# Kernel tuning notes

Hardware: AMD Instinct MI355X
Metric: run time of the kernel (lower is better)

The kernel has to match this reference:

```python
import jax, jax.numpy as jnp
import numpy as np

NUM_BINS = 16
TAIL_BOUND = 3.0
MIN_BIN_WIDTH = 1e-3
MIN_BIN_HEIGHT = 1e-3
MIN_DERIVATIVE = 1e-3
DERIV_CONST = float(np.log(np.exp(1.0 - MIN_DERIVATIVE) - 1.0))  # softplus^-1(1-min_d)

FEATURES = 512
BATCH = 8192
HIDDEN = 1024


def setup_inputs() -> dict:
    key = jax.random.key(0)
    k1, k2, k3 = jax.random.split(key, 3)
    n_id = FEATURES // 2
    n_tr = FEATURES // 2
    out_dim = n_tr * (3 * NUM_BINS - 1)  # 47 params per transformed feature
    inputs = jax.random.normal(k1, (BATCH, FEATURES), jnp.float32)
    W1 = jax.random.normal(k2, (n_id, HIDDEN), jnp.float32) * (1.0 / np.sqrt(n_id))
    b1 = jnp.zeros((HIDDEN,), jnp.float32)
    W2 = jax.random.normal(k3, (HIDDEN, out_dim), jnp.float32) * (1.0 / np.sqrt(HIDDEN))
    b2 = jnp.zeros((out_dim,), jnp.float32)
    # mask = [1,0,1,0,...]: transform features at even indices, identity at odd
    transform_idx = jnp.arange(0, FEATURES, 2, dtype=jnp.int32)
    identity_idx = jnp.arange(1, FEATURES, 2, dtype=jnp.int32)
    return dict(inputs=inputs, W1=W1, b1=b1, W2=W2, b2=b2,
                identity_idx=identity_idx, transform_idx=transform_idx)


def _rq_spline_forward(x, uw, uh, ud):
    """Unconstrained (linear-tail) rational-quadratic spline, forward direction.
    x: [B, D]; uw/uh: [B, D, K]; ud: [B, D, K-1]. Returns (y, logabsdet) per-element."""
    K = NUM_BINS
    B_ = TAIL_BOUND
    inside = (x >= -B_) & (x <= B_)
    xc = jnp.clip(x, -B_, B_)  # safe values for gather/formula; masked out later

    # pad derivatives with the constant so boundary derivative == 1 (linear tails)
    pad = jnp.full(ud.shape[:-1] + (1,), DERIV_CONST, ud.dtype)
    ud = jnp.concatenate([pad, ud, pad], axis=-1)  # [B, D, K+1]

    widths = jax.nn.softmax(uw, axis=-1)
    widths = MIN_BIN_WIDTH + (1.0 - MIN_BIN_WIDTH * K) * widths
    cumw = jnp.cumsum(widths, axis=-1)
    cumw = jnp.pad(cumw, [(0, 0), (0, 0), (1, 0)])
    cumw = 2.0 * B_ * cumw - B_
    cumw = cumw.at[..., 0].set(-B_).at[..., -1].set(B_)
    widths = jnp.diff(cumw, axis=-1)

    heights = jax.nn.softmax(uh, axis=-1)
    heights = MIN_BIN_HEIGHT + (1.0 - MIN_BIN_HEIGHT * K) * heights
    cumh = jnp.cumsum(heights, axis=-1)
    cumh = jnp.pad(cumh, [(0, 0), (0, 0), (1, 0)])
    cumh = 2.0 * B_ * cumh - B_
    cumh = cumh.at[..., 0].set(-B_).at[..., -1].set(B_)
    heights = jnp.diff(cumh, axis=-1)

    derivs = MIN_DERIVATIVE + jax.nn.softplus(ud)  # [B, D, K+1]
    delta = heights / widths                        # [B, D, K]

    # data-dependent bin search (searchsorted equivalent)
    idx = jnp.clip(jnp.sum((xc[..., None] >= cumw).astype(jnp.int32), axis=-1) - 1, 0, K - 1)
    idx = idx[..., None]
    g = lambda a: jnp.take_along_axis(a, idx, axis=-1)[..., 0]

    in_cw, in_w = g(cumw), g(widths)
    in_ch, in_h = g(cumh), g(heights)
    in_delta = g(delta)
    d0 = g(derivs)
    d1 = jnp.take_along_axis(derivs, idx + 1, axis=-1)[..., 0]

    theta = (xc - in_cw) / in_w
    t1m = theta * (1.0 - theta)
    denom = in_delta + (d0 + d1 - 2.0 * in_delta) * t1m
    numer = in_h * (in_delta * theta * theta + d0 * t1m)
    y = in_ch + numer / denom
    dnum = in_delta * in_delta * (d1 * theta * theta + 2.0 * in_delta * t1m + d0 * (1.0 - theta) ** 2)
    lad = jnp.log(dnum) - 2.0 * jnp.log(denom)

    y = jnp.where(inside, y, x)          # linear tails: identity outside
    lad = jnp.where(inside, lad, 0.0)
    return y, lad


def reference(inputs, W1, b1, W2, b2, identity_idx, transform_idx):
    B = inputs.shape[0]
    n_tr = transform_idx.shape[0]
    K = NUM_BINS
    identity_split = inputs[:, identity_idx]      # [B, 256]
    transform_split = inputs[:, transform_idx]    # [B, 256]

    h = jax.nn.relu(identity_split @ W1 + b1)
    params = (h @ W2 + b2).reshape(B, n_tr, 3 * K - 1)
    uw = params[..., :K]
    uh = params[..., K:2 * K]
    ud = params[..., 2 * K:]

    y, lad = _rq_spline_forward(transform_split, uw, uh, ud)
    logabsdet = jnp.sum(lad, axis=-1)  # sum_except_batch

    outputs = jnp.zeros_like(inputs)
    outputs = outputs.at[:, identity_idx].set(identity_split)
    outputs = outputs.at[:, transform_idx].set(y)
    return outputs, logabsdet
```

## Files before the change

### kernel.cpp

```cpp
#include <hip/hip_runtime.h>

#define BATCH 8192
#define FEAT  512
#define NID   256
#define NTR   256
#define HID   1024
#define PPF   47
#define PPFP  48
#define NOUT  (NTR*PPF)
#define TBOUND 3.0f
#define MIN_W 0.001f
#define MIN_H 0.001f
#define MIN_D 0.001f

typedef __bf16 bf16x8 __attribute__((ext_vector_type(8)));
typedef float  f32x4  __attribute__((ext_vector_type(4)));

__device__ __forceinline__ unsigned short f2bf(float f) {
  unsigned u = __float_as_uint(f);
  u += 0x7FFFu + ((u >> 16) & 1u);
  return (unsigned short)(u >> 16);
}

__device__ __forceinline__ void gload16(const void* g, void* l) {
  __builtin_amdgcn_global_load_lds(
      (const __attribute__((address_space(1))) void*)g,
      (__attribute__((address_space(3))) void*)l, 16, 0, 0);
}

__global__ void k_pack_all(const float* __restrict__ in,
                           const float* __restrict__ W1,
                           const float* __restrict__ W2,
                           unsigned short* __restrict__ idbf,
                           unsigned short* __restrict__ W1T,
                           unsigned short* __restrict__ W2T,
                           float* __restrict__ outp) {
  const int bid = blockIdx.x;
  const int tid = threadIdx.x;
  if (bid < 4096) {
    int b = bid * 2 + (tid >> 7);
    int j4 = tid & 127;
    float4 v = ((const float4*)(in + (long)b * FEAT))[j4];
    ((float4*)(outp + (long)b * FEAT))[j4] = v;
    ushort2 h;
    h.x = f2bf(v.y);
    h.y = f2bf(v.w);
    ((ushort2*)(idbf + (long)b * NID))[j4] = h;
  } else if (bid < 4160) {
    __shared__ unsigned short tl[64][65];
    int i = bid - 4096;
    int n0 = (i & 15) * 64, k0 = (i >> 4) * 64;
    int c = tid & 63, r4 = tid >> 6;
    #pragma unroll
    for (int j = 0; j < 16; ++j) {
      int kk = r4 + j * 4;
      tl[kk][c] = f2bf(W1[(k0 + kk) * HID + n0 + c]);
    }
    __syncthreads();
    #pragma unroll
    for (int j = 0; j < 16; ++j) {
      int nn = r4 + j * 4;
      W1T[(n0 + nn) * NID + k0 + c] = tl[c][nn];
    }
  } else if (bid < 7168) {
    __shared__ unsigned short tl[64][65];
    int i = bid - 4160;
    int ns0 = (i % 188) * 64, k0 = (i / 188) * 64;
    int c = tid & 63, r4 = tid >> 6;
    #pragma unroll
    for (int j = 0; j < 16; ++j) {
      int kk = r4 + j * 4;
      tl[kk][c] = f2bf(W2[(k0 + kk) * (long)NOUT + ns0 + c]);
    }
    __syncthreads();
    #pragma unroll
    for (int j = 0; j < 16; ++j) {
      int nn = r4 + j * 4;
      int ns = ns0 + nn;
      int nd = (ns / PPF) * PPFP + (ns % PPF);
      W2T[(long)nd * HID + k0 + c] = tl[c][nn];
    }
  } else {
    int idx = (bid - 7168) * 256 + tid;
    int f = idx >> 10, k = idx & 1023;
    W2T[((long)(f * PPFP + PPF)) * HID + k] = 0;
  }
}

__global__ __launch_bounds__(256, 2) void k_gemm1(
    const unsigned short* __restrict__ A, const unsigned short* __restrict__ Bw,
    const float* __restrict__ b1, unsigned short* __restrict__ H) {
  __shared__ __align__(16) char sm[65536];
  const int tid = threadIdx.x;
  const int lane = tid & 63, wid = tid >> 6;
  const int c = lane & 15, g = lane >> 4;
  const int wm = wid >> 1, wn = wid & 1;
  const int m0 = blockIdx.x * 128, n0 = blockIdx.y * 128;

  f32x4 zero = {0.f, 0.f, 0.f, 0.f};
  f32x4 acc[4][4];
  #pragma unroll
  for (int a = 0; a < 4; ++a)
    #pragma unroll
    for (int b = 0; b < 4; ++b) acc[a][b] = zero;

  #define G1_STAGE(half, ks)                                                   \
    {                                                                          \
      char* bA = sm + (half) * 32768;                                          \
      char* bB = bA + 16384;                                                   \
      _Pragma("unroll")                                                        \
      for (int j = 0; j < 4; ++j) {                                            \
        int s0 = j * 256 + wid * 64;                                           \
        int s = s0 + lane;                                                     \
        int row = s >> 3, kb = (s & 7) ^ (row & 7);                            \
        gload16(A + (long)(m0 + row) * NID + (ks) * 64 + kb * 8, bA + s0 * 16);\
        gload16(Bw + (long)(n0 + row) * NID + (ks) * 64 + kb * 8, bB + s0 * 16);\
      }                                                                        \
    }

  G1_STAGE(0, 0);
  __syncthreads();
  for (int ks = 0; ks < 4; ++ks) {
    int cur = ks & 1;
    if (ks < 3) G1_STAGE(cur ^ 1, ks + 1);
    char* bA = sm + cur * 32768;
    char* bB = bA + 16384;
    #pragma unroll
    for (int kk = 0; kk < 2; ++kk) {
      bf16x8 av[4], bv[4];
      int kbl = kk * 4 + g;
      #pragma unroll
      for (int mf = 0; mf < 4; ++mf) {
        int row = wm * 64 + mf * 16 + c;
        av[mf] = *(const bf16x8*)(bA + row * 128 + ((kbl ^ (row & 7)) << 4));
      }
      #pragma unroll
      for (int nf = 0; nf < 4; ++nf) {
        int col = wn * 64 + nf * 16 + c;
        bv[nf] = *(const bf16x8*)(bB + col * 128 + ((kbl ^ (col & 7)) << 4));
      }
      #pragma unroll
      for (int mf = 0; mf < 4; ++mf)
        #pragma unroll
        for (int nf = 0; nf < 4; ++nf)
          acc[mf][nf] = __builtin_amdgcn_mfma_f32_16x16x32_bf16(
              av[mf], bv[nf], acc[mf][nf], 0, 0, 0);
    }
    __syncthreads();
  }
  #pragma unroll
  for (int nf = 0; nf < 4; ++nf) {
    float bb = b1[n0 + wn * 64 + nf * 16 + c];
    #pragma unroll
    for (int mf = 0; mf < 4; ++mf) {
      #pragma unroll
      for (int i = 0; i < 4; ++i) {
        int row = m0 + wm * 64 + mf * 16 + 4 * g + i;
        int col = n0 + wn * 64 + nf * 16 + c;
        float v = acc[mf][nf][i] + bb;
        H[(long)row * HID + col] = f2bf(fmaxf(v, 0.f));
      }
    }
  }
}

__global__ __launch_bounds__(512, 4) void k_gemm2_spline(
    const unsigned short* __restrict__ Hb, const unsigned short* __restrict__ W2T,
    const float* __restrict__ b2, const float* __restrict__ inp,
    float* __restrict__ outp, float* __restrict__ ladw) {
  __shared__ __align__(16) char sm[81920];
  const int tid = threadIdx.x;
  const int lane = tid & 63, wid = tid >> 6;
  const int c = lane & 15, g = lane >> 4;
  const int wm = wid >> 2, wn = wid & 3;
  const long m0 = (long)blockIdx.x * 128;
  const int bn = blockIdx.y;
  const int n0 = bn * 192;

  f32x4 zero = {0.f, 0.f, 0.f, 0.f};
  f32x4 acc[4][3];
  #pragma unroll
  for (int a = 0; a < 4; ++a)
    #pragma unroll
    for (int b = 0; b < 3; ++b) acc[a][b] = zero;

  const char *gA0, *gA1, *gB0, *gB1, *gB2;
  int dA0, dA1, dB0, dB1, dB2;
  {
    int s0, s, row, kb;
    s0 = wid * 64;            s = s0 + lane; row = s >> 3; kb = (s & 7) ^ (row & 7);
    gA0 = (const char*)(Hb + (m0 + row) * 1024L + kb * 8); dA0 = s0 * 16;
    s0 = 512 + wid * 64;      s = s0 + lane; row = s >> 3; kb = (s & 7) ^ (row & 7);
    gA1 = (const char*)(Hb + (m0 + row) * 1024L + kb * 8); dA1 = s0 * 16;
    s0 = wid * 64;            s = s0 + lane; row = s >> 3; kb = (s & 7) ^ (row & 7);
    gB0 = (const char*)(W2T + (long)(n0 + row) * 1024L + kb * 8); dB0 = s0 * 16 + 16384;
    s0 = 512 + wid * 64;      s = s0 + lane; row = s >> 3; kb = (s & 7) ^ (row & 7);
    gB1 = (const char*)(W2T + (long)(n0 + row) * 1024L + kb * 8); dB1 = s0 * 16 + 16384;
    s0 = 1024 + wid * 64;     s = s0 + lane; row = s >> 3; kb = (s & 7) ^ (row & 7);
    gB2 = (const char*)(W2T + (long)(n0 + row) * 1024L + kb * 8); dB2 = s0 * 16 + 16384;
  }
  int oA[2][4], oB[2][3];
  #pragma unroll
  for (int kk = 0; kk < 2; ++kk) {
    int kbl = kk * 4 + g;
    #pragma unroll
    for (int mf = 0; mf < 4; ++mf) {
      int row = wm * 64 + mf * 16 + c;
      oA[kk][mf] = row * 128 + ((kbl ^ (row & 7)) << 4);
    }
    #pragma unroll
    for (int nf = 0; nf < 3; ++nf) {
      int col = wn * 48 + nf * 16 + c;
      oB[kk][nf] = col * 128 + ((kbl ^ (col & 7)) << 4) + 16384;
    }
  }

  #define G2_STAGE(HALF, IMM)                                        \
    {                                                                \
      gload16(gA0 + (IMM), sm + (HALF) * 40960 + dA0);               \
      gload16(gA1 + (IMM), sm + (HALF) * 40960 + dA1);               \
      gload16(gB0 + (IMM), sm + (HALF) * 40960 + dB0);               \
      gload16(gB1 + (IMM), sm + (HALF) * 40960 + dB1);               \
      gload16(gB2 + (IMM), sm + (HALF) * 40960 + dB2);               \
    }

  #define G2_BUMP(N) { gA0 += (N); gA1 += (N); gB0 += (N); gB1 += (N); gB2 += (N); }

  #define G2_COMP(HALF)                                                        \
    {                                                                          \
      _Pragma("unroll")                                                        \
      for (int kk = 0; kk < 2; ++kk) {                                         \
        bf16x8 av[4], bv[3];                                                   \
        _Pragma("unroll")                                                      \
        for (int mf = 0; mf < 4; ++mf)                                         \
          av[mf] = *(const bf16x8*)(sm + (HALF) * 40960 + oA[kk][mf]);         \
        _Pragma("unroll")                                                      \
        for (int nf = 0; nf < 3; ++nf)                                         \
          bv[nf] = *(const bf16x8*)(sm + (HALF) * 40960 + oB[kk][nf]);         \
        _Pragma("unroll")                                                      \
        for (int mf = 0; mf < 4; ++mf)                                         \
          _Pragma("unroll")                                                    \
          for (int nf = 0; nf < 3; ++nf)                                       \
            acc[mf][nf] = __builtin_amdgcn_mfma_f32_16x16x32_bf16(             \
                av[mf], bv[nf], acc[mf][nf], 0, 0, 0);                         \
      }                                                                        \
    }

  G2_STAGE(0, 0);
  G2_BUMP(128);
  __syncthreads();
  for (int ks2 = 0; ks2 < 7; ++ks2) {
    G2_STAGE(1, 0);
    G2_COMP(0);
    __syncthreads();
    G2_STAGE(0, 128);
    G2_COMP(1);
    __syncthreads();
    G2_BUMP(256);
  }
  G2_STAGE(1, 0);
  G2_COMP(0);
  __syncthreads();
  G2_COMP(1);
  __syncthreads();

  float* stA = (float*)(sm + wid * 8704);
  float* stB = stA + 1088;
  const int t = bn * 4 + wn;
  const float* b2t = b2 + t * PPF;
  const float bw = b2t[c];
  const float bh = b2t[16 + c];
  const float bd = (c < 15) ? b2t[32 + c] : 0.f;
  const long r = m0 + wm * 64 + lane;
  float x = inp[r * FEAT + 2 * t];

  #pragma unroll
  for (int mf = 0; mf < 4; ++mf) {
    f32x4 vw = acc[mf][0], vh = acc[mf][1];
    #pragma unroll
    for (int i = 0; i < 4; ++i) { vw[i] += bw; vh[i] += bh; }
    *(f32x4*)(stA + c * 68 + mf * 16 + 4 * g) = vw;
    *(f32x4*)(stB + c * 68 + mf * 16 + 4 * g) = vh;
  }

  float xc = fminf(fmaxf(x, -TBOUND), TBOUND);
  int idx = 0;
  float in_cw, in_w, in_ch, in_h;
  {
    float u[16];
    #pragma unroll
    for (int k = 0; k < 16; ++k) u[k] = stA[k * 68 + lane];
    float mx = u[0];
    #pragma unroll
    for (int k = 1; k < 16; ++k) mx = fmaxf(mx, u[k]);
    float e[16], s = 0.f;
    #pragma unroll
    for (int k = 0; k < 16; ++k) { e[k] = __expf(u[k] - mx); s += e[k]; }
    float inv = (1.f - MIN_W * 16.f) / s;
    float wk = fmaf(e[0], inv, MIN_W);
    float wsel = wk, cum = 0.f;
    in_cw = -TBOUND;
    #pragma unroll
    for (int k = 0; k < 15; ++k) {
      cum += wk;
      float knot = fmaf(2.f * TBOUND, cum, -TBOUND);
      float wk1 = fmaf(e[k + 1], inv, MIN_W);
      bool le = (knot <= xc);
      idx = le ? k + 1 : idx;
      in_cw = le ? knot : in_cw;
      wsel = le ? wk1 : wsel;
      wk = wk1;
    }
    in_w = 2.f * TBOUND * wsel;
  }
  #pragma unroll
  for (int mf = 0; mf < 4; ++mf) {
    f32x4 vd = acc[mf][2];
    #pragma unroll
    for (int i = 0; i < 4; ++i) vd[i] += bd;
    *(f32x4*)(stA + c * 68 + mf * 16 + 4 * g) = vd;
  }
  {
    float u[16];
    #pragma unroll
    for (int k = 0; k < 16; ++k) u[k] = stB[k * 68 + lane];
    float mx = u[0];
    #pragma unroll
    for (int k = 1; k < 16; ++k) mx = fmaxf(mx, u[k]);
    float e[16], s = 0.f;
    #pragma unroll
    for (int k = 0; k < 16; ++k) { e[k] = __expf(u[k] - mx); s += e[k]; }
    float inv = (1.f - MIN_H * 16.f) / s;
    float hk = fmaf(e[0], inv, MIN_H);
    float hsel = hk, cum = 0.f;
    in_ch = -TBOUND;
    #pragma unroll
    for (int k = 0; k < 15; ++k) {
      cum += hk;
      float knot = fmaf(2.f * TBOUND, cum, -TBOUND);
      float hk1 = fmaf(e[k + 1], inv, MIN_H);
      bool pick = (idx == k + 1);
      in_ch = pick ? knot : in_ch;
      hsel = pick ? hk1 : hsel;
      hk = hk1;
    }
    in_h = 2.f * TBOUND * hsel;
  }
  float d0, d1;
  {
    int i0 = (idx > 0) ? idx - 1 : 0;
    int i1 = (idx < 15) ? idx : 14;
    float v0 = stA[i0 * 68 + lane];
    float v1 = stA[i1 * 68 + lane];
    float sp0 = (v0 > 0.f) ? (v0 + log1pf(__expf(-v0))) : log1pf(__expf(v0));
    float sp1 = (v1 > 0.f) ? (v1 + log1pf(__expf(-v1))) : log1pf(__expf(v1));
    d0 = (idx == 0) ? 1.f : (MIN_D + sp0);
    d1 = (idx == 15) ? 1.f : (MIN_D + sp1);
  }
  float dlt = in_h / in_w;
  float th = (xc - in_cw) / in_w;
  float omt = 1.f - th, t1m = th * omt;
  float den = dlt + (d0 + d1 - 2.f * dlt) * t1m;
  float num = in_h * (dlt * th * th + d0 * t1m);
  float y = in_ch + num / den;
  float dn = dlt * dlt * (d1 * th * th + 2.f * dlt * t1m + d0 * omt * omt);
  float lad = __logf(dn) - 2.f * __logf(den);
  bool inside = (x >= -TBOUND) && (x <= TBOUND);
  y = inside ? y : x;
  lad = inside ? lad : 0.f;
  outp[r * FEAT + 2 * t] = y;
  ladw[r * NTR + t] = lad;
}

__global__ void k_reduce_lad(const float* __restrict__ ladw,
                             float* __restrict__ lado) {
  int wid = threadIdx.x >> 6, lane = threadIdx.x & 63;
  long b = (long)blockIdx.x * 4 + wid;
  const float4* p = (const float4*)(ladw + b * NTR);
  float4 v = p[lane];
  float s = v.x + v.y + v.z + v.w;
  #pragma unroll
  for (int d = 1; d < 64; d <<= 1) s += __shfl_xor(s, d, 64);
  if (lane == 0) lado[b] = s;
}

extern "C" void kernel_launch(void* const* d_in, const int* in_sizes, int n_in,
                              void* d_out, int out_size, void* d_ws, size_t ws_size,
                              hipStream_t stream) {
  const float* inp = (const float*)d_in[0];
  const float* W1  = (const float*)d_in[1];
  const float* b1  = (const float*)d_in[2];
  const float* W2  = (const float*)d_in[3];
  const float* b2  = (const float*)d_in[4];
  float* outp = (float*)d_out;
  float* lado = outp + (long)BATCH * FEAT;

  char* ws = (char*)d_ws;
  unsigned short* Hb   = (unsigned short*)(ws);
  unsigned short* idbf = (unsigned short*)(ws + 16777216);
  unsigned short* W1T  = (unsigned short*)(ws + 20971520);
  unsigned short* W2T  = (unsigned short*)(ws + 21495808);
  float*          ladw = (float*)(ws + 46661632);

  k_pack_all<<<dim3(8192), dim3(256), 0, stream>>>(inp, W1, W2, idbf, W1T, W2T, outp);
  k_gemm1<<<dim3(64, 8), dim3(256), 0, stream>>>(idbf, W1T, b1, Hb);
  k_gemm2_spline<<<dim3(64, 64), dim3(512), 0, stream>>>(Hb, W2T, b2, inp, outp, ladw);
  k_reduce_lad<<<dim3(2048), dim3(256), 0, stream>>>(ladw, lado);
}
```

Measured before the change: 228.9 us.

## Fuse logabsdet reduction into spline kernel and write identity features there

```diff
diff --git a/kernel.cpp b/kernel.cpp
--- a/kernel.cpp
+++ b/kernel.cpp
@@ -34,18 +34,21 @@
                            unsigned short* __restrict__ idbf,
                            unsigned short* __restrict__ W1T,
                            unsigned short* __restrict__ W2T,
-                           float* __restrict__ outp) {
+                           float* __restrict__ lado) {
   const int bid = blockIdx.x;
   const int tid = threadIdx.x;
   if (bid < 4096) {
     int b = bid * 2 + (tid >> 7);
     int j4 = tid & 127;
     float4 v = ((const float4*)(in + (long)b * FEAT))[j4];
-    ((float4*)(outp + (long)b * FEAT))[j4] = v;
     ushort2 h;
     h.x = f2bf(v.y);
     h.y = f2bf(v.w);
     ((ushort2*)(idbf + (long)b * NID))[j4] = h;
+    if (tid == 0) {
+      lado[2 * bid] = 0.f;
+      lado[2 * bid + 1] = 0.f;
+    }
   } else if (bid < 4160) {
     __shared__ unsigned short tl[64][65];
     int i = bid - 4096;
@@ -167,7 +170,7 @@
 __global__ __launch_bounds__(512, 4) void k_gemm2_spline(
     const unsigned short* __restrict__ Hb, const unsigned short* __restrict__ W2T,
     const float* __restrict__ b2, const float* __restrict__ inp,
-    float* __restrict__ outp, float* __restrict__ ladw) {
+    float* __restrict__ outp, float* __restrict__ lado) {
   __shared__ __align__(16) char sm[81920];
   const int tid = threadIdx.x;
   const int lane = tid & 63, wid = tid >> 6;
@@ -272,7 +275,8 @@
   const float bh = b2t[16 + c];
   const float bd = (c < 15) ? b2t[32 + c] : 0.f;
   const long r = m0 + wm * 64 + lane;
-  float x = inp[r * FEAT + 2 * t];
+  float2 x2 = *(const float2*)(inp + r * FEAT + 2 * t);
+  const float x = x2.x;
 
   #pragma unroll
   for (int mf = 0; mf < 4; ++mf) {
@@ -368,20 +372,17 @@
   bool inside = (x >= -TBOUND) && (x <= TBOUND);
   y = inside ? y : x;
   lad = inside ? lad : 0.f;
-  outp[r * FEAT + 2 * t] = y;
-  ladw[r * NTR + t] = lad;
-}
-
-__global__ void k_reduce_lad(const float* __restrict__ ladw,
-                             float* __restrict__ lado) {
-  int wid = threadIdx.x >> 6, lane = threadIdx.x & 63;
-  long b = (long)blockIdx.x * 4 + wid;
-  const float4* p = (const float4*)(ladw + b * NTR);
-  float4 v = p[lane];
-  float s = v.x + v.y + v.z + v.w;
-  #pragma unroll
-  for (int d = 1; d < 64; d <<= 1) s += __shfl_xor(s, d, 64);
-  if (lane == 0) lado[b] = s;
+  float2 o; o.x = y; o.y = x2.y;
+  *(float2*)(outp + r * FEAT + 2 * t) = o;
+
+  float* ldr = (float*)(sm + 71680);
+  ldr[(wm * 64 + lane) * 5 + wn] = lad;
+  __syncthreads();
+  if (tid < 128) {
+    float s = ldr[tid * 5 + 0] + ldr[tid * 5 + 1] +
+              ldr[tid * 5 + 2] + ldr[tid * 5 + 3];
+    atomicAdd(&lado[m0 + tid], s);
+  }
 }
 
 extern "C" void kernel_launch(void* const* d_in, const int* in_sizes, int n_in,
@@ -400,10 +401,8 @@
   unsigned short* idbf = (unsigned short*)(ws + 16777216);
   unsigned short* W1T  = (unsigned short*)(ws + 20971520);
   unsigned short* W2T  = (unsigned short*)(ws + 21495808);
-  float*          ladw = (float*)(ws + 46661632);
-
-  k_pack_all<<<dim3(8192), dim3(256), 0, stream>>>(inp, W1, W2, idbf, W1T, W2T, outp);
+
+  k_pack_all<<<dim3(8192), dim3(256), 0, stream>>>(inp, W1, W2, idbf, W1T, W2T, lado);
   k_gemm1<<<dim3(64, 8), dim3(256), 0, stream>>>(idbf, W1T, b1, Hb);
-  k_gemm2_spline<<<dim3(64, 64), dim3(512), 0, stream>>>(Hb, W2T, b2, inp, outp, ladw);
-  k_reduce_lad<<<dim3(2048), dim3(256), 0, stream>>>(ladw, lado);
-}
+  k_gemm2_spline<<<dim3(64, 64), dim3(512), 0, stream>>>(Hb, W2T, b2, inp, outp, lado);
+}
```

After: 223.5 us. 1.02x faster.
